# Kernel tuning notes

Hardware: AMD Instinct MI355X
Metric: run time of the kernel (lower is better)

Reference implementation:

```python
import jax, jax.numpy as jnp
import numpy as np

D_MODEL = 4096
D_FIBER = 16
D_CONTROL = 64
EMA_MOMENTUM = 0.9


def setup_inputs() -> dict:
    key = jax.random.key(0)
    k_h, k_f, k_w1, k_w2 = jax.random.split(key, 4)
    B, S = 4, 2048
    hidden = jax.random.normal(k_h, (B, S, D_MODEL), dtype=jnp.float32)
    # torch nn.Linear stores weight as [out, in]; fiber_proj init: normal std=0.02
    W_fiber = jax.random.normal(k_f, (D_FIBER, D_MODEL), dtype=jnp.float32) * 0.02
    # predictor[0]: Linear(d_model+d_fiber, d_control) with default torch init (uniform)
    fan_in1 = D_MODEL + D_FIBER
    bound1 = 1.0 / np.sqrt(fan_in1)
    W1 = jax.random.uniform(k_w1, (D_CONTROL, fan_in1), dtype=jnp.float32, minval=-bound1, maxval=bound1)
    b1 = jnp.zeros((D_CONTROL,), dtype=jnp.float32)
    # predictor[-2]: Linear(d_control, 1), weight normal std=0.01, bias zero
    W2 = jax.random.normal(k_w2, (1, D_CONTROL), dtype=jnp.float32) * 0.01
    b2 = jnp.zeros((1,), dtype=jnp.float32)
    lam = jnp.asarray(1.0, dtype=jnp.float32)
    return {"hidden": hidden, "W_fiber": W_fiber, "W1": W1, "b1": b1, "W2": W2, "b2": b2, "lam": lam}


def _causal_ema(delta_h, alpha):
    # h_t = alpha*h_{t-1} + (1-alpha)*d_t, h_{-1} = 0. delta_h: [B,S]
    B = delta_h.shape[0]
    def step(h_prev, d_t):
        h_t = alpha * h_prev + (1.0 - alpha) * d_t
        return h_t, h_t
    _, hs = jax.lax.scan(step, jnp.zeros((B,), delta_h.dtype), jnp.swapaxes(delta_h, 0, 1))
    return jnp.swapaxes(hs, 0, 1)  # [B,S]


def reference(hidden, W_fiber, W1, b1, W2, b2, lam):
    h = hidden.astype(jnp.float32)                      # [B,S,D]
    fiber = jnp.einsum('bsd,fd->bsf', h, W_fiber)       # [B,S,16]
    combined = jnp.concatenate([h, fiber], axis=-1)     # [B,S,D+16]
    z = jax.nn.gelu(jnp.einsum('bsc,kc->bsk', combined, W1) + b1, approximate=False)
    delta_h = jax.nn.softplus(jnp.einsum('bsk,ok->bso', z, W2) + b2)[..., 0]  # [B,S]
    field = _causal_ema(delta_h, EMA_MOMENTUM)          # [B,S]
    gate = jax.nn.sigmoid(-lam * field)
    return gate.astype(hidden.dtype), field.astype(hidden.dtype), delta_h.mean()
```

## Files before the change

kernel.cpp:

```cpp
#include <hip/hip_runtime.h>
#include <hip/hip_bf16.h>

#define D_MODEL 4096
#define NTOK    8192
#define SEQ     2048

typedef short bf16x8 __attribute__((ext_vector_type(8)));
typedef float f32x4  __attribute__((ext_vector_type(4)));

__device__ __forceinline__ short f2bf(float x) {
  __hip_bfloat16 h = __float2bfloat16(x);
  return *reinterpret_cast<short*>(&h);
}
__device__ __forceinline__ float bfs2f(unsigned short u) {
  unsigned int x = ((unsigned int)u) << 16;
  float f;
  __builtin_memcpy(&f, &x, 4);
  return f;
}
__device__ __forceinline__ float bf2f(const void* p, size_t i) {
  return bfs2f(((const unsigned short*)p)[i]);
}

__device__ __forceinline__ int sniff_wave(const unsigned short* p, int n) {
  int lane = threadIdx.x & 63;
  int S = n / 2 < 64 ? n / 2 : 64;
  bool act = lane < S;
  unsigned short ve = 0, vo = 0;
  if (act) { ve = p[2 * lane]; vo = p[2 * lane + 1]; }
  int ee = (ve >> 7) & 0xFF, eo = (vo >> 7) & 0xFF;
  bool ve_band   = (ve == 0) || (ve == 0x8000) || (ee >= 96 && ee <= 141);
  bool vo_bandnz = (vo != 0) && (vo != 0x8000) && (eo >= 96 && eo <= 141);
  int zp = __popcll(__ballot(act && ve == 0 && vo == 0));
  int ob = __popcll(__ballot(act && ve == 0 && vo_bandnz));
  int eb = __popcll(__ballot(act && ve_band));
  if (zp == S) return 1;
  if (4 * ob >= 3 * S) return 0;
  if (4 * eb >= 3 * S) return 1;
  return 0;
}

__device__ __forceinline__ float decode_lam(const void* lamp) {
  unsigned short l0 = *(const unsigned short*)lamp;
  int le = (l0 >> 7) & 0xFF;
  if (l0 != 0 && l0 != 0x8000 && le >= 96 && le <= 141)
    return bfs2f(l0);
  return *(const float*)lamp;
}
__device__ __forceinline__ float decode_b2(const void* p) {
  unsigned short c0 = *(const unsigned short*)p;
  int ce = (c0 >> 7) & 0xFF;
  if (c0 == 0) return 0.0f;
  if (c0 != 0x8000 && ce >= 96 && ce <= 141)
    return bfs2f(c0);
  return *(const float*)p;
}

__global__ __launch_bounds__(256) void fold_w1(const void* __restrict__ W1v,
                                               const void* __restrict__ Wfv,
                                               short* __restrict__ W1eff) {
  int n = blockIdx.x;
  int fw1 = sniff_wave((const unsigned short*)W1v, 64 * 4112);
  int fwf = sniff_wave((const unsigned short*)Wfv, 16 * D_MODEL);
  __shared__ float w1b[16];
  if (threadIdx.x < 16) {
    size_t idx = (size_t)n * 4112 + 4096 + threadIdx.x;
    w1b[threadIdx.x] = fw1 ? bf2f(W1v, idx) : ((const float*)W1v)[idx];
  }
  __syncthreads();
  for (int it = 0; it < 4; ++it) {
    int k0 = it * 1024 + threadIdx.x * 4;
    size_t idx = (size_t)n * 4112 + k0;
    float v0, v1, v2, v3;
    if (fw1) {
      ushort4 u = *(const ushort4*)((const unsigned short*)W1v + idx);
      v0 = bfs2f(u.x); v1 = bfs2f(u.y); v2 = bfs2f(u.z); v3 = bfs2f(u.w);
    } else {
      float4 f = *(const float4*)((const float*)W1v + idx);
      v0 = f.x; v1 = f.y; v2 = f.z; v3 = f.w;
    }
#pragma unroll
    for (int f = 0; f < 16; ++f) {
      size_t wi = (size_t)f * D_MODEL + k0;
      float w0, w1_, w2_, w3_;
      if (fwf) {
        ushort4 u = *(const ushort4*)((const unsigned short*)Wfv + wi);
        w0 = bfs2f(u.x); w1_ = bfs2f(u.y); w2_ = bfs2f(u.z); w3_ = bfs2f(u.w);
      } else {
        float4 fv = *(const float4*)((const float*)Wfv + wi);
        w0 = fv.x; w1_ = fv.y; w2_ = fv.z; w3_ = fv.w;
      }
      float s = w1b[f];
      v0 += s * w0; v1 += s * w1_; v2 += s * w2_; v3 += s * w3_;
    }
    ushort4 o;
    o.x = (unsigned short)f2bf(v0); o.y = (unsigned short)f2bf(v1);
    o.z = (unsigned short)f2bf(v2); o.w = (unsigned short)f2bf(v3);
    *(ushort4*)(W1eff + (size_t)n * D_MODEL + k0) = o;
  }
}

__global__ __launch_bounds__(512, 4) void gemm_stream(const void* __restrict__ hid,
                                                      const short* __restrict__ B_,
                                                      const void* __restrict__ b1,
                                                      const void* __restrict__ w2,
                                                      const void* __restrict__ b2,
                                                      float* __restrict__ delta) {
  int t = blockIdx.x;
  int w = threadIdx.x >> 6, lane = threadIdx.x & 63;
  int m = lane & 15, kg = lane >> 4;

  __shared__ float red[8][16][68];

  int fhid = sniff_wave((const unsigned short*)hid, NTOK * D_MODEL);

  f32x4 acc0 = {0.f, 0.f, 0.f, 0.f};
  f32x4 acc1 = acc0, acc2 = acc0, acc3 = acc0;

  size_t abase = (size_t)(t * 16 + m) * D_MODEL + w * 512 + kg * 8;
  const short* Bp = B_ + (size_t)m * D_MODEL + w * 512 + kg * 8;

  if (fhid) {
    const short* Ap = (const short*)hid + abase;
    bf16x8 ar[2], br[2][4];
#pragma unroll
    for (int p = 0; p < 2; ++p) {
      ar[p] = *(const bf16x8*)(Ap + p * 32);
#pragma unroll
      for (int nc = 0; nc < 4; ++nc)
        br[p][nc] = *(const bf16x8*)(Bp + (size_t)nc * 16 * D_MODEL + p * 32);
    }
#pragma unroll
    for (int s = 0; s < 16; ++s) {
      int cur = s & 1;
      bf16x8 a  = ar[cur];
      bf16x8 f0 = br[cur][0], f1 = br[cur][1], f2 = br[cur][2], f3 = br[cur][3];
      if (s + 2 < 16) {
        ar[cur] = *(const bf16x8*)(Ap + (s + 2) * 32);
#pragma unroll
        for (int nc = 0; nc < 4; ++nc)
          br[cur][nc] = *(const bf16x8*)(Bp + (size_t)nc * 16 * D_MODEL + (s + 2) * 32);
      }
      acc0 = __builtin_amdgcn_mfma_f32_16x16x32_bf16(a, f0, acc0, 0, 0, 0);
      acc1 = __builtin_amdgcn_mfma_f32_16x16x32_bf16(a, f1, acc1, 0, 0, 0);
      acc2 = __builtin_amdgcn_mfma_f32_16x16x32_bf16(a, f2, acc2, 0, 0, 0);
      acc3 = __builtin_amdgcn_mfma_f32_16x16x32_bf16(a, f3, acc3, 0, 0, 0);
    }
  } else {
    const float* Ap = (const float*)hid + abase;
    for (int s = 0; s < 16; ++s) {
      float4 lo = *(const float4*)(Ap + s * 32);
      float4 hi = *(const float4*)(Ap + s * 32 + 4);
      bf16x8 a;
      a[0] = f2bf(lo.x); a[1] = f2bf(lo.y); a[2] = f2bf(lo.z); a[3] = f2bf(lo.w);
      a[4] = f2bf(hi.x); a[5] = f2bf(hi.y); a[6] = f2bf(hi.z); a[7] = f2bf(hi.w);
#pragma unroll
      for (int nc = 0; nc < 4; ++nc) {
        bf16x8 bb = *(const bf16x8*)(Bp + (size_t)nc * 16 * D_MODEL + s * 32);
        if (nc == 0) acc0 = __builtin_amdgcn_mfma_f32_16x16x32_bf16(a, bb, acc0, 0, 0, 0);
        if (nc == 1) acc1 = __builtin_amdgcn_mfma_f32_16x16x32_bf16(a, bb, acc1, 0, 0, 0);
        if (nc == 2) acc2 = __builtin_amdgcn_mfma_f32_16x16x32_bf16(a, bb, acc2, 0, 0, 0);
        if (nc == 3) acc3 = __builtin_amdgcn_mfma_f32_16x16x32_bf16(a, bb, acc3, 0, 0, 0);
      }
    }
  }

#pragma unroll
  for (int r = 0; r < 4; ++r) {
    int tok = kg * 4 + r;
    red[w][tok][m +  0] = acc0[r];
    red[w][tok][m + 16] = acc1[r];
    red[w][tok][m + 32] = acc2[r];
    red[w][tok][m + 48] = acc3[r];
  }
  __syncthreads();

  if (threadIdx.x < 256) {
    int tok = threadIdx.x >> 4;
    int cid = threadIdx.x & 15;
    int fb1 = sniff_wave((const unsigned short*)b1, 64);
    int fw2 = sniff_wave((const unsigned short*)w2, 64);
    float y = 0.f;
#pragma unroll
    for (int j = 0; j < 4; ++j) {
      int col = cid + 16 * j;
      float s = 0.f;
#pragma unroll
      for (int q = 0; q < 8; ++q) s += red[q][tok][col];
      s += fb1 ? bf2f(b1, col) : ((const float*)b1)[col];
      float g = 0.5f * s * (1.0f + erff(s * 0.70710678118654752f));
      y += g * (fw2 ? bf2f(w2, col) : ((const float*)w2)[col]);
    }
#pragma unroll
    for (int off = 1; off <= 8; off <<= 1) y += __shfl_xor(y, off, 64);
    if (cid == 0) {
      float x = y + decode_b2(b2);
      float d = (x > 20.0f) ? x : log1pf(expf(x));
      delta[t * 16 + tok] = d;
    }
  }
}

__global__ __launch_bounds__(256) void ema_out(const float* __restrict__ delta,
                                               const void* __restrict__ lamp,
                                               float* __restrict__ out) {
  int b    = threadIdx.x >> 6;
  int lane = threadIdx.x & 63;
  const float alpha = 0.9f;
  float d[32];
  const float* dp = delta + b * SEQ + lane * 32;
  float beta = 0.f, lsum = 0.f;
#pragma unroll
  for (int i = 0; i < 32; ++i) {
    d[i] = dp[i];
    lsum += d[i];
    beta = alpha * beta + 0.1f * d[i];
  }
  float accA = 0.03433683820292512f;
  float accB = beta;
  for (int off = 1; off < 64; off <<= 1) {
    float uA = __shfl_up(accA, off, 64);
    float uB = __shfl_up(accB, off, 64);
    if (lane >= off) {
      accB = accB + accA * uB;
      accA = accA * uA;
    }
  }
  float prev = __shfl_up(accB, 1, 64);
  float h = (lane == 0) ? 0.f : prev;
  float lam = decode_lam(lamp);
#pragma unroll
  for (int i = 0; i < 32; ++i) {
    h = alpha * h + 0.1f * d[i];
    float gate = 1.0f / (1.0f + expf(lam * h));
    out[b * SEQ + lane * 32 + i]        = gate;
    out[NTOK + b * SEQ + lane * 32 + i] = h;
  }
#pragma unroll
  for (int off = 32; off >= 1; off >>= 1) lsum += __shfl_xor(lsum, off, 64);
  __shared__ float bs[4];
  if (lane == 0) bs[b] = lsum;
  __syncthreads();
  if (threadIdx.x == 0)
    out[2 * NTOK] = (bs[0] + bs[1] + bs[2] + bs[3]) * (1.0f / 8192.0f);
}

extern "C" void kernel_launch(void* const* d_in, const int* in_sizes, int n_in,
                              void* d_out, int out_size, void* d_ws, size_t ws_size,
                              hipStream_t stream) {
  const void* hidden = d_in[0];
  const void* Wf     = d_in[1];
  const void* W1     = d_in[2];
  const void* b1     = d_in[3];
  const void* W2     = d_in[4];
  const void* b2     = d_in[5];
  const void* lam    = d_in[6];
  float* out = (float*)d_out;

  char* ws = (char*)d_ws;
  short* W1eff = (short*)ws;
  float* delta = (float*)(ws + (size_t)64 * D_MODEL * 2);

  fold_w1<<<64, 256, 0, stream>>>(W1, Wf, W1eff);
  gemm_stream<<<512, 512, 0, stream>>>(hidden, W1eff, b1, W2, b2, delta);
  ema_out<<<1, 256, 0, stream>>>(delta, lam, out);
}
```

Measured before the change: 237.2 us.

## Stage bf16 hidden tiles in LDS via direct global-to-LDS loads with swizzle

Adds a new bf16 GEMM path that copies 16-token hidden tiles straight into a 64KB double-buffered, XOR-swizzled LDS buffer using global_load_lds. Each wave then reads its A fragments from LDS instead of issuing its own global loads. The per-wave K split is changed to interleaved 128-element chunks in both paths, and the reduction scratch now reuses the same shared buffer. The larger LDS footprint can lower occupancy. The fp32 input path, which the sniff heuristic likely selects for these float32 inputs, only gets a reordered K traversal and an extra barrier.

```diff
diff --git a/kernel.cpp b/kernel.cpp
--- a/kernel.cpp
+++ b/kernel.cpp
@@ -20,6 +20,12 @@
 }
 __device__ __forceinline__ float bf2f(const void* p, size_t i) {
   return bfs2f(((const unsigned short*)p)[i]);
+}
+
+__device__ __forceinline__ void gload_lds16(const void* g, void* l) {
+  __builtin_amdgcn_global_load_lds(
+      (__attribute__((address_space(1))) void*)(g),
+      (__attribute__((address_space(3))) void*)(l), 16, 0, 0);
 }
 
 __device__ __forceinline__ int sniff_wave(const unsigned short* p, int n) {
@@ -100,78 +106,110 @@
   }
 }
 
-__global__ __launch_bounds__(512, 4) void gemm_stream(const void* __restrict__ hid,
-                                                      const short* __restrict__ B_,
-                                                      const void* __restrict__ b1,
-                                                      const void* __restrict__ w2,
-                                                      const void* __restrict__ b2,
-                                                      float* __restrict__ delta) {
+__global__ __launch_bounds__(512, 4) void gemm_lds(const void* __restrict__ hid,
+                                                   const short* __restrict__ B_,
+                                                   const void* __restrict__ b1,
+                                                   const void* __restrict__ w2,
+                                                   const void* __restrict__ b2,
+                                                   float* __restrict__ delta) {
   int t = blockIdx.x;
   int w = threadIdx.x >> 6, lane = threadIdx.x & 63;
   int m = lane & 15, kg = lane >> 4;
 
-  __shared__ float red[8][16][68];
+  __shared__ char smem[65536];
 
   int fhid = sniff_wave((const unsigned short*)hid, NTOK * D_MODEL);
 
   f32x4 acc0 = {0.f, 0.f, 0.f, 0.f};
   f32x4 acc1 = acc0, acc2 = acc0, acc3 = acc0;
 
-  size_t abase = (size_t)(t * 16 + m) * D_MODEL + w * 512 + kg * 8;
-  const short* Bp = B_ + (size_t)m * D_MODEL + w * 512 + kg * 8;
+  const short* Bp = B_ + (size_t)m * D_MODEL + kg * 8;
 
   if (fhid) {
-    const short* Ap = (const short*)hid + abase;
-    bf16x8 ar[2], br[2][4];
+    bf16x8 br[2][4];
 #pragma unroll
     for (int p = 0; p < 2; ++p) {
-      ar[p] = *(const bf16x8*)(Ap + p * 32);
+      int ko = (p >> 2) * 1024 + w * 128 + (p & 3) * 32;
 #pragma unroll
       for (int nc = 0; nc < 4; ++nc)
-        br[p][nc] = *(const bf16x8*)(Bp + (size_t)nc * 16 * D_MODEL + p * 32);
-    }
-#pragma unroll
-    for (int s = 0; s < 16; ++s) {
-      int cur = s & 1;
-      bf16x8 a  = ar[cur];
-      bf16x8 f0 = br[cur][0], f1 = br[cur][1], f2 = br[cur][2], f3 = br[cur][3];
-      if (s + 2 < 16) {
-        ar[cur] = *(const bf16x8*)(Ap + (s + 2) * 32);
-#pragma unroll
-        for (int nc = 0; nc < 4; ++nc)
-          br[cur][nc] = *(const bf16x8*)(Bp + (size_t)nc * 16 * D_MODEL + (s + 2) * 32);
+        br[p][nc] = *(const bf16x8*)(Bp + (size_t)nc * 16 * D_MODEL + ko);
+    }
+#pragma unroll
+    for (int j = 0; j < 4; ++j) {
+      int dloc = w * 4096 + j * 1024 + lane * 16;
+      int row  = dloc >> 11;
+      int cb0  = (dloc & 2047) ^ ((row & 7) << 4);
+      const char* g = (const char*)hid +
+          ((size_t)(t * 16 + row) * D_MODEL) * 2 + cb0;
+      gload_lds16(g, smem + (w * 4096 + j * 1024));
+    }
+    __syncthreads();
+
+#pragma unroll
+    for (int c = 0; c < 4; ++c) {
+      int buf = c & 1;
+      if (c < 3) {
+#pragma unroll
+        for (int j = 0; j < 4; ++j) {
+          int dloc = w * 4096 + j * 1024 + lane * 16;
+          int row  = dloc >> 11;
+          int cb0  = (dloc & 2047) ^ ((row & 7) << 4);
+          const char* g = (const char*)hid +
+              ((size_t)(t * 16 + row) * D_MODEL + (size_t)(c + 1) * 1024) * 2 + cb0;
+          gload_lds16(g, smem + ((buf ^ 1) * 32768 + w * 4096 + j * 1024));
+        }
       }
-      acc0 = __builtin_amdgcn_mfma_f32_16x16x32_bf16(a, f0, acc0, 0, 0, 0);
-      acc1 = __builtin_amdgcn_mfma_f32_16x16x32_bf16(a, f1, acc1, 0, 0, 0);
-      acc2 = __builtin_amdgcn_mfma_f32_16x16x32_bf16(a, f2, acc2, 0, 0, 0);
-      acc3 = __builtin_amdgcn_mfma_f32_16x16x32_bf16(a, f3, acc3, 0, 0, 0);
+#pragma unroll
+      for (int s = 0; s < 4; ++s) {
+        int g = c * 4 + s;
+        int cb = w * 256 + s * 64 + kg * 16;
+        bf16x8 a = *(const bf16x8*)(smem + buf * 32768 + m * 2048 +
+                                    (cb ^ ((m & 7) << 4)));
+        int cur = g & 1;
+        bf16x8 f0 = br[cur][0], f1 = br[cur][1], f2 = br[cur][2], f3 = br[cur][3];
+        if (g + 2 < 16) {
+          int ko = ((g + 2) >> 2) * 1024 + w * 128 + ((g + 2) & 3) * 32;
+#pragma unroll
+          for (int nc = 0; nc < 4; ++nc)
+            br[cur][nc] = *(const bf16x8*)(Bp + (size_t)nc * 16 * D_MODEL + ko);
+        }
+        acc0 = __builtin_amdgcn_mfma_f32_16x16x32_bf16(a, f0, acc0, 0, 0, 0);
+        acc1 = __builtin_amdgcn_mfma_f32_16x16x32_bf16(a, f1, acc1, 0, 0, 0);
+        acc2 = __builtin_amdgcn_mfma_f32_16x16x32_bf16(a, f2, acc2, 0, 0, 0);
+        acc3 = __builtin_amdgcn_mfma_f32_16x16x32_bf16(a, f3, acc3, 0, 0, 0);
+      }
+      __syncthreads();
     }
   } else {
-    const float* Ap = (const float*)hid + abase;
-    for (int s = 0; s < 16; ++s) {
-      float4 lo = *(const float4*)(Ap + s * 32);
-      float4 hi = *(const float4*)(Ap + s * 32 + 4);
+    const float* Ap = (const float*)hid + (size_t)(t * 16 + m) * D_MODEL + kg * 8;
+    for (int g = 0; g < 16; ++g) {
+      int ko = (g >> 2) * 1024 + w * 128 + (g & 3) * 32;
+      float4 lo = *(const float4*)(Ap + ko);
+      float4 hi = *(const float4*)(Ap + ko + 4);
       bf16x8 a;
       a[0] = f2bf(lo.x); a[1] = f2bf(lo.y); a[2] = f2bf(lo.z); a[3] = f2bf(lo.w);
       a[4] = f2bf(hi.x); a[5] = f2bf(hi.y); a[6] = f2bf(hi.z); a[7] = f2bf(hi.w);
 #pragma unroll
       for (int nc = 0; nc < 4; ++nc) {
-        bf16x8 bb = *(const bf16x8*)(Bp + (size_t)nc * 16 * D_MODEL + s * 32);
+        bf16x8 bb = *(const bf16x8*)(Bp + (size_t)nc * 16 * D_MODEL + ko);
         if (nc == 0) acc0 = __builtin_amdgcn_mfma_f32_16x16x32_bf16(a, bb, acc0, 0, 0, 0);
         if (nc == 1) acc1 = __builtin_amdgcn_mfma_f32_16x16x32_bf16(a, bb, acc1, 0, 0, 0);
         if (nc == 2) acc2 = __builtin_amdgcn_mfma_f32_16x16x32_bf16(a, bb, acc2, 0, 0, 0);
         if (nc == 3) acc3 = __builtin_amdgcn_mfma_f32_16x16x32_bf16(a, bb, acc3, 0, 0, 0);
       }
     }
-  }
-
+    __syncthreads();
+  }
+
+  float* redf = (float*)smem;
 #pragma unroll
   for (int r = 0; r < 4; ++r) {
     int tok = kg * 4 + r;
-    red[w][tok][m +  0] = acc0[r];
-    red[w][tok][m + 16] = acc1[r];
-    red[w][tok][m + 32] = acc2[r];
-    red[w][tok][m + 48] = acc3[r];
+    float* rp = redf + (size_t)(w * 16 + tok) * 68;
+    rp[m +  0] = acc0[r];
+    rp[m + 16] = acc1[r];
+    rp[m + 32] = acc2[r];
+    rp[m + 48] = acc3[r];
   }
   __syncthreads();
 
@@ -186,7 +224,7 @@
       int col = cid + 16 * j;
       float s = 0.f;
 #pragma unroll
-      for (int q = 0; q < 8; ++q) s += red[q][tok][col];
+      for (int q = 0; q < 8; ++q) s += redf[(size_t)(q * 16 + tok) * 68 + col];
       s += fb1 ? bf2f(b1, col) : ((const float*)b1)[col];
       float g = 0.5f * s * (1.0f + erff(s * 0.70710678118654752f));
       y += g * (fw2 ? bf2f(w2, col) : ((const float*)w2)[col]);
@@ -262,6 +300,6 @@
   float* delta = (float*)(ws + (size_t)64 * D_MODEL * 2);
 
   fold_w1<<<64, 256, 0, stream>>>(W1, Wf, W1eff);
-  gemm_stream<<<512, 512, 0, stream>>>(hidden, W1eff, b1, W2, b2, delta);
+  gemm_lds<<<512, 512, 0, stream>>>(hidden, W1eff, b1, W2, b2, delta);
   ema_out<<<1, 256, 0, stream>>>(delta, lam, out);
 }
```

After: 233.5 us. No clear change (-1.5%).

## Split GEMM by K-chunk with LDS-staged weights and separate epilogue kernel

Applied to the files above, without the earlier changes.

Each GEMM block now handles 128 tokens over one 512-wide K chunk. It stages the matching weight slice into swizzled LDS with global_load_lds and preloads all A fragments into registers, instead of every wave re-reading the weights from global memory. Partial sums for the eight K chunks go to a workspace buffer, and a new epilogue kernel reduces them and applies GELU, the W2 dot product and softplus. Weight reuse improves, but the cost is an extra kernel launch and roughly 16 MB of partial-sum traffic written and read back.

```diff
diff --git a/kernel.cpp b/kernel.cpp
--- a/kernel.cpp
+++ b/kernel.cpp
@@ -20,6 +20,12 @@
 }
 __device__ __forceinline__ float bf2f(const void* p, size_t i) {
   return bfs2f(((const unsigned short*)p)[i]);
+}
+
+__device__ __forceinline__ void gload_lds16(const void* g, void* l) {
+  __builtin_amdgcn_global_load_lds(
+      (__attribute__((address_space(1))) void*)(g),
+      (__attribute__((address_space(3))) void*)(l), 16, 0, 0);
 }
 
 __device__ __forceinline__ int sniff_wave(const unsigned short* p, int n) {
@@ -100,104 +106,112 @@
   }
 }
 
-__global__ __launch_bounds__(512, 4) void gemm_stream(const void* __restrict__ hid,
-                                                      const short* __restrict__ B_,
-                                                      const void* __restrict__ b1,
-                                                      const void* __restrict__ w2,
-                                                      const void* __restrict__ b2,
-                                                      float* __restrict__ delta) {
-  int t = blockIdx.x;
-  int w = threadIdx.x >> 6, lane = threadIdx.x & 63;
+__global__ __launch_bounds__(512, 4) void gemm_part(const void* __restrict__ hid,
+                                                    const short* __restrict__ B_,
+                                                    float* __restrict__ part) {
+  int c = blockIdx.x >> 6;
+  int t = blockIdx.x & 63;
+  int w    = threadIdx.x >> 6;
+  int lane = threadIdx.x & 63;
   int m = lane & 15, kg = lane >> 4;
 
-  __shared__ float red[8][16][68];
+  __shared__ short Bs[64 * 512];
 
   int fhid = sniff_wave((const unsigned short*)hid, NTOK * D_MODEL);
+
+#pragma unroll
+  for (int i = 0; i < 8; ++i) {
+    int n = w * 8 + i;
+    const char* src = (const char*)(B_ + (size_t)n * D_MODEL + c * 512) +
+                      ((lane ^ (n & 7)) * 16);
+    gload_lds16(src, (char*)Bs + n * 1024);
+  }
 
   f32x4 acc0 = {0.f, 0.f, 0.f, 0.f};
   f32x4 acc1 = acc0, acc2 = acc0, acc3 = acc0;
-
-  size_t abase = (size_t)(t * 16 + m) * D_MODEL + w * 512 + kg * 8;
-  const short* Bp = B_ + (size_t)m * D_MODEL + w * 512 + kg * 8;
+  size_t abase = (size_t)(t * 128 + w * 16 + m) * D_MODEL + c * 512 + kg * 8;
 
   if (fhid) {
     const short* Ap = (const short*)hid + abase;
-    bf16x8 ar[2], br[2][4];
-#pragma unroll
-    for (int p = 0; p < 2; ++p) {
-      ar[p] = *(const bf16x8*)(Ap + p * 32);
-#pragma unroll
-      for (int nc = 0; nc < 4; ++nc)
-        br[p][nc] = *(const bf16x8*)(Bp + (size_t)nc * 16 * D_MODEL + p * 32);
-    }
+    bf16x8 areg[16];
+#pragma unroll
+    for (int i = 0; i < 16; ++i) areg[i] = *(const bf16x8*)(Ap + i * 32);
+    __syncthreads();
 #pragma unroll
     for (int s = 0; s < 16; ++s) {
-      int cur = s & 1;
-      bf16x8 a  = ar[cur];
-      bf16x8 f0 = br[cur][0], f1 = br[cur][1], f2 = br[cur][2], f3 = br[cur][3];
-      if (s + 2 < 16) {
-        ar[cur] = *(const bf16x8*)(Ap + (s + 2) * 32);
-#pragma unroll
-        for (int nc = 0; nc < 4; ++nc)
-          br[cur][nc] = *(const bf16x8*)(Bp + (size_t)nc * 16 * D_MODEL + (s + 2) * 32);
-      }
-      acc0 = __builtin_amdgcn_mfma_f32_16x16x32_bf16(a, f0, acc0, 0, 0, 0);
-      acc1 = __builtin_amdgcn_mfma_f32_16x16x32_bf16(a, f1, acc1, 0, 0, 0);
-      acc2 = __builtin_amdgcn_mfma_f32_16x16x32_bf16(a, f2, acc2, 0, 0, 0);
-      acc3 = __builtin_amdgcn_mfma_f32_16x16x32_bf16(a, f3, acc3, 0, 0, 0);
+      int u  = s * 4 + kg;
+      int sw = (u ^ (m & 7)) * 16;
+      bf16x8 b0 = *(const bf16x8*)((const char*)Bs + (m +  0) * 1024 + sw);
+      bf16x8 b1 = *(const bf16x8*)((const char*)Bs + (m + 16) * 1024 + sw);
+      bf16x8 b2 = *(const bf16x8*)((const char*)Bs + (m + 32) * 1024 + sw);
+      bf16x8 b3 = *(const bf16x8*)((const char*)Bs + (m + 48) * 1024 + sw);
+      acc0 = __builtin_amdgcn_mfma_f32_16x16x32_bf16(areg[s], b0, acc0, 0, 0, 0);
+      acc1 = __builtin_amdgcn_mfma_f32_16x16x32_bf16(areg[s], b1, acc1, 0, 0, 0);
+      acc2 = __builtin_amdgcn_mfma_f32_16x16x32_bf16(areg[s], b2, acc2, 0, 0, 0);
+      acc3 = __builtin_amdgcn_mfma_f32_16x16x32_bf16(areg[s], b3, acc3, 0, 0, 0);
     }
   } else {
     const float* Ap = (const float*)hid + abase;
+    __syncthreads();
     for (int s = 0; s < 16; ++s) {
       float4 lo = *(const float4*)(Ap + s * 32);
       float4 hi = *(const float4*)(Ap + s * 32 + 4);
       bf16x8 a;
       a[0] = f2bf(lo.x); a[1] = f2bf(lo.y); a[2] = f2bf(lo.z); a[3] = f2bf(lo.w);
       a[4] = f2bf(hi.x); a[5] = f2bf(hi.y); a[6] = f2bf(hi.z); a[7] = f2bf(hi.w);
-#pragma unroll
-      for (int nc = 0; nc < 4; ++nc) {
-        bf16x8 bb = *(const bf16x8*)(Bp + (size_t)nc * 16 * D_MODEL + s * 32);
-        if (nc == 0) acc0 = __builtin_amdgcn_mfma_f32_16x16x32_bf16(a, bb, acc0, 0, 0, 0);
-        if (nc == 1) acc1 = __builtin_amdgcn_mfma_f32_16x16x32_bf16(a, bb, acc1, 0, 0, 0);
-        if (nc == 2) acc2 = __builtin_amdgcn_mfma_f32_16x16x32_bf16(a, bb, acc2, 0, 0, 0);
-        if (nc == 3) acc3 = __builtin_amdgcn_mfma_f32_16x16x32_bf16(a, bb, acc3, 0, 0, 0);
-      }
-    }
-  }
-
+      int u  = s * 4 + kg;
+      int sw = (u ^ (m & 7)) * 16;
+      bf16x8 b0 = *(const bf16x8*)((const char*)Bs + (m +  0) * 1024 + sw);
+      bf16x8 b1 = *(const bf16x8*)((const char*)Bs + (m + 16) * 1024 + sw);
+      bf16x8 b2 = *(const bf16x8*)((const char*)Bs + (m + 32) * 1024 + sw);
+      bf16x8 b3 = *(const bf16x8*)((const char*)Bs + (m + 48) * 1024 + sw);
+      acc0 = __builtin_amdgcn_mfma_f32_16x16x32_bf16(a, b0, acc0, 0, 0, 0);
+      acc1 = __builtin_amdgcn_mfma_f32_16x16x32_bf16(a, b1, acc1, 0, 0, 0);
+      acc2 = __builtin_amdgcn_mfma_f32_16x16x32_bf16(a, b2, acc2, 0, 0, 0);
+      acc3 = __builtin_amdgcn_mfma_f32_16x16x32_bf16(a, b3, acc3, 0, 0, 0);
+    }
+  }
+
+  float* po = part + ((size_t)c * NTOK + (size_t)t * 128 + w * 16) * 64;
 #pragma unroll
   for (int r = 0; r < 4; ++r) {
-    int tok = kg * 4 + r;
-    red[w][tok][m +  0] = acc0[r];
-    red[w][tok][m + 16] = acc1[r];
-    red[w][tok][m + 32] = acc2[r];
-    red[w][tok][m + 48] = acc3[r];
-  }
-  __syncthreads();
-
-  if (threadIdx.x < 256) {
-    int tok = threadIdx.x >> 4;
-    int cid = threadIdx.x & 15;
-    int fb1 = sniff_wave((const unsigned short*)b1, 64);
-    int fw2 = sniff_wave((const unsigned short*)w2, 64);
-    float y = 0.f;
-#pragma unroll
-    for (int j = 0; j < 4; ++j) {
-      int col = cid + 16 * j;
-      float s = 0.f;
-#pragma unroll
-      for (int q = 0; q < 8; ++q) s += red[q][tok][col];
-      s += fb1 ? bf2f(b1, col) : ((const float*)b1)[col];
-      float g = 0.5f * s * (1.0f + erff(s * 0.70710678118654752f));
-      y += g * (fw2 ? bf2f(w2, col) : ((const float*)w2)[col]);
-    }
-#pragma unroll
-    for (int off = 1; off <= 8; off <<= 1) y += __shfl_xor(y, off, 64);
-    if (cid == 0) {
-      float x = y + decode_b2(b2);
-      float d = (x > 20.0f) ? x : log1pf(expf(x));
-      delta[t * 16 + tok] = d;
-    }
+    int row = kg * 4 + r;
+    po[row * 64 + (m +  0)] = acc0[r];
+    po[row * 64 + (m + 16)] = acc1[r];
+    po[row * 64 + (m + 32)] = acc2[r];
+    po[row * 64 + (m + 48)] = acc3[r];
+  }
+}
+
+__global__ __launch_bounds__(256) void delta_ep(const float* __restrict__ part,
+                                                const void* __restrict__ b1,
+                                                const void* __restrict__ w2,
+                                                const void* __restrict__ b2p,
+                                                float* __restrict__ delta) {
+  int t   = blockIdx.x & 63;
+  int sub = blockIdx.x >> 6;
+  int tok = t * 128 + sub * 16 + (threadIdx.x >> 4);
+  int cid = threadIdx.x & 15;
+  int fb1 = sniff_wave((const unsigned short*)b1, 64);
+  int fw2 = sniff_wave((const unsigned short*)w2, 64);
+  float y = 0.f;
+#pragma unroll
+  for (int j = 0; j < 4; ++j) {
+    int col = cid + 16 * j;
+    float s = 0.f;
+#pragma unroll
+    for (int c = 0; c < 8; ++c)
+      s += part[((size_t)c * NTOK + tok) * 64 + col];
+    s += fb1 ? bf2f(b1, col) : ((const float*)b1)[col];
+    float g = 0.5f * s * (1.0f + erff(s * 0.70710678118654752f));
+    y += g * (fw2 ? bf2f(w2, col) : ((const float*)w2)[col]);
+  }
+#pragma unroll
+  for (int off = 1; off <= 8; off <<= 1) y += __shfl_xor(y, off, 64);
+  if (cid == 0) {
+    float x = y + decode_b2(b2p);
+    float d = (x > 20.0f) ? x : log1pf(expf(x));
+    delta[tok] = d;
   }
 }
 
@@ -260,8 +274,10 @@
   char* ws = (char*)d_ws;
   short* W1eff = (short*)ws;
   float* delta = (float*)(ws + (size_t)64 * D_MODEL * 2);
+  float* part  = (float*)(ws + (size_t)64 * D_MODEL * 2 + NTOK * 4);
 
   fold_w1<<<64, 256, 0, stream>>>(W1, Wf, W1eff);
-  gemm_stream<<<512, 512, 0, stream>>>(hidden, W1eff, b1, W2, b2, delta);
+  gemm_part<<<512, 512, 0, stream>>>(hidden, W1eff, part);
+  delta_ep<<<512, 256, 0, stream>>>(part, b1, W2, b2, delta);
   ema_out<<<1, 256, 0, stream>>>(delta, lam, out);
 }
```

New measurement: 230.8 us. 1.03x faster.
